# Kernel optimization log

Hardware: AMD Instinct MI355X
Metric: run time of the kernel (lower is better)

The kernel has to match this reference:

```python
import jax, jax.numpy as jnp
import numpy as np

B, S, HIDDEN = 2, 2048, 2048
H, KVH, HD = 16, 4, 128
N_REP = H // KVH
WIN = 3  # hardcoded window_size in the module
ROPE_THETA = 10000.0


def _rope(x, cos, sin):
    # x: [b, s, h, d]; cos/sin: [s, d//2]. Pairs are consecutive elements
    # (view_as_complex on reshape(..., -1, 2)): a = even idx, b = odd idx.
    a = x[..., 0::2]
    b = x[..., 1::2]
    c = cos[None, :, None, :]
    s = sin[None, :, None, :]
    out = jnp.stack([a * c - b * s, a * s + b * c], axis=-1)  # [b,s,h,d//2,2]
    return out.reshape(x.shape)


def setup_inputs() -> dict:
    key = jax.random.key(0)
    ks = jax.random.split(key, 5)
    x = jax.random.normal(ks[0], (B, S, HIDDEN), dtype=jnp.float32)
    scale = 0.02
    wq = jax.random.normal(ks[1], (HIDDEN, H * HD), dtype=jnp.float32) * scale
    wk = jax.random.normal(ks[2], (HIDDEN, KVH * HD), dtype=jnp.float32) * scale
    wv = jax.random.normal(ks[3], (HIDDEN, KVH * HD), dtype=jnp.float32) * scale
    wo = jax.random.normal(ks[4], (H * HD, HIDDEN), dtype=jnp.float32) * scale
    # Standard RoPE angles (equivalent to the complex freqs_cis)
    inv_freq = 1.0 / (ROPE_THETA ** (np.arange(0, HD, 2, dtype=np.float64) / HD))
    ang = np.outer(np.arange(S, dtype=np.float64), inv_freq)  # [S, HD//2]
    cos = jnp.asarray(np.cos(ang), dtype=jnp.float32)
    sin = jnp.asarray(np.sin(ang), dtype=jnp.float32)
    return {"x": x, "wq": wq, "wk": wk, "wv": wv, "wo": wo, "cos": cos, "sin": sin}


def reference(x, wq, wk, wv, wo, cos, sin):
    q = (x @ wq).reshape(B, S, H, HD)
    k = (x @ wk).reshape(B, S, KVH, HD)
    v = (x @ wv).reshape(B, S, KVH, HD)
    q = _rope(q, cos, sin)
    k = _rope(k, cos, sin)
    # GQA: repeat kv heads (repeat_kv)
    k = jnp.repeat(k, N_REP, axis=2)  # [B,S,H,HD]
    v = jnp.repeat(v, N_REP, axis=2)
    scores = jnp.einsum("bqhd,bkhd->bhqk", q, k) / np.float32(np.sqrt(HD))
    i = jnp.arange(S)[:, None]
    j = jnp.arange(S)[None, :]
    allowed = (j <= i) & (j > i - WIN)
    scores = jnp.where(allowed, scores, -jnp.inf)
    attn = jax.nn.softmax(scores.astype(jnp.float32), axis=-1).astype(q.dtype)
    out = jnp.einsum("bhqk,bkhd->bqhd", attn, v).reshape(B, S, H * HD)
    return (out @ wo, attn)
```

## Files before the change

### kernel.cpp

```cpp
#include <hip/hip_runtime.h>

#define SEQ 2048
#define HID 2048
#define NH 16
#define NKVH 4
#define HDIM 128
#define NB 2
#define MTOT (NB * SEQ)
#define QKV_N (NH * HDIM + 2 * NKVH * HDIM)
#define OUT0_ELEMS (NB * SEQ * HID)
#define ATTN_ELEMS ((size_t)NB * NH * SEQ * SEQ)
#define Z1_CHUNK 26048
#define Z1_TOTAL ((long)768 * Z1_CHUNK)
#define Z2_CHUNK 26464

typedef __bf16 bf16x8 __attribute__((ext_vector_type(8)));
typedef float f32x4 __attribute__((ext_vector_type(4)));

__device__ __forceinline__ unsigned short f2bf(float f) {
  unsigned int u = __float_as_uint(f);
  u += 0x7FFFu + ((u >> 16) & 1u);
  return (unsigned short)(u >> 16);
}
__device__ __forceinline__ float bf2f(unsigned short u) {
  return __uint_as_float(((unsigned int)u) << 16);
}

__global__ __launch_bounds__(256) void prep_k(
    const float* __restrict__ x, const float* __restrict__ wq,
    const float* __restrict__ wk, const float* __restrict__ wv,
    const float* __restrict__ wo, unsigned short* __restrict__ Xbf,
    unsigned short* __restrict__ Wqkvt, unsigned short* __restrict__ Wot) {
  __shared__ float tile[32][33];
  const int bid = blockIdx.x, t = threadIdx.x;
  if (bid < 8192) {
    int i = bid * 256 + t;
    float4 v = ((const float4*)x)[i];
    ushort4 o;
    o.x = f2bf(v.x); o.y = f2bf(v.y); o.z = f2bf(v.z); o.w = f2bf(v.w);
    ((ushort4*)Xbf)[i] = o;
    return;
  }
  int lb = bid - 8192;
  const float* W; unsigned short* Wt; int gx, N;
  if (lb < 4096)      { W = wq; Wt = Wqkvt;                       gx = 64; N = 2048; }
  else if (lb < 5120) { W = wk; Wt = Wqkvt + (size_t)2048 * HID;  gx = 16; N = 512;  lb -= 4096; }
  else if (lb < 6144) { W = wv; Wt = Wqkvt + (size_t)2560 * HID;  gx = 16; N = 512;  lb -= 5120; }
  else                { W = wo; Wt = Wot;                         gx = 64; N = 2048; lb -= 6144; }
  const int n0 = (lb % gx) * 32, k0 = (lb / gx) * 32;
  const int tx = t & 31, ty = t >> 5;
  #pragma unroll
  for (int r = 0; r < 32; r += 8)
    tile[ty + r][tx] = W[(size_t)(k0 + ty + r) * N + n0 + tx];
  __syncthreads();
  #pragma unroll
  for (int r = 0; r < 32; r += 8)
    Wt[(size_t)(n0 + ty + r) * HID + k0 + tx] = f2bf(tile[tx][ty + r]);
}

template <bool OUT_BF16>
__global__ __launch_bounds__(256) void gemm_bt_k(
    const unsigned short* __restrict__ A, const unsigned short* __restrict__ Bt,
    void* __restrict__ Cv, int M, int N, int K,
    f32x4* __restrict__ attn4, long zoff, int zchunk) {
  __shared__ unsigned short As[128 * 64];
  __shared__ unsigned short Bs[128 * 64];
  const int t = threadIdx.x;
  const int nbx = gridDim.x;
  const int rawbid = blockIdx.y * nbx + blockIdx.x;
  const int nwg = nbx * gridDim.y;
  const int sw = (rawbid & 7) * (nwg >> 3) + (rawbid >> 3);
  const int row0 = (sw / nbx) << 7;
  const int col0 = (sw % nbx) << 7;
  const int lane = t & 63;
  const int wave = t >> 6;
  const int wr = (wave >> 1) << 6;
  const int wc = (wave & 1) << 6;
  const int lrow = lane & 15;
  const int kofs = (lane >> 4) << 3;

  const long zbase = zoff + (long)rawbid * zchunk;

  f32x4 acc[4][4];
  #pragma unroll
  for (int a = 0; a < 4; ++a)
    #pragma unroll
    for (int b = 0; b < 4; ++b)
      #pragma unroll
      for (int r = 0; r < 4; ++r) acc[a][b][r] = 0.f;

  const unsigned short* Ab = A + (size_t)row0 * K;
  const unsigned short* Bb = Bt + (size_t)col0 * K;

  const int nk = K >> 6;
  for (int kt = 0; kt < nk; ++kt) {
    const int k0 = kt << 6;
    if (kt) __syncthreads();
    #pragma unroll
    for (int i = 0; i < 4; ++i) {
      const int c = i * 256 + t;
      const int row = c >> 3, c8 = (c & 7) << 3;
      __builtin_amdgcn_global_load_lds(
          (const __attribute__((address_space(1))) void*)(Ab + (size_t)row * K + k0 + c8),
          (__attribute__((address_space(3))) void*)(As + c * 8), 16, 0, 0);
      __builtin_amdgcn_global_load_lds(
          (const __attribute__((address_space(1))) void*)(Bb + (size_t)row * K + k0 + c8),
          (__attribute__((address_space(3))) void*)(Bs + c * 8), 16, 0, 0);
    }
    __syncthreads();

    #pragma unroll
    for (int s = 0; s < 4; ++s) {
      int il = (kt * 4 + s) * 256 + t;
      if (il < zchunk) {
        long g = zbase + il;
        int c = (int)(g & 511);
        int i = (int)((g >> 9) & (SEQ - 1));
        int hi = i >> 2;
        int lo = (i >= 2 ? i - 2 : 0) >> 2;
        if (c != hi && c != lo) {
          f32x4 z = {0.f, 0.f, 0.f, 0.f};
          __builtin_nontemporal_store(z, attn4 + g);
        }
      }
    }

    #pragma unroll
    for (int ks = 0; ks < 2; ++ks) {
      bf16x8 af[4], bfr[4];
      #pragma unroll
      for (int mf = 0; mf < 4; ++mf)
        af[mf] = *(const bf16x8*)(As + ((wr + mf * 16 + lrow) << 6) + (ks << 5) + kofs);
      #pragma unroll
      for (int nf = 0; nf < 4; ++nf)
        bfr[nf] = *(const bf16x8*)(Bs + ((wc + nf * 16 + lrow) << 6) + (ks << 5) + kofs);
      #pragma unroll
      for (int mf = 0; mf < 4; ++mf)
        #pragma unroll
        for (int nf = 0; nf < 4; ++nf)
          acc[mf][nf] = __builtin_amdgcn_mfma_f32_16x16x32_bf16(af[mf], bfr[nf],
                                                                acc[mf][nf], 0, 0, 0);
    }
  }

  const int cr = row0 + wr + ((lane >> 4) << 2);
  const int cc = col0 + wc + (lane & 15);
  #pragma unroll
  for (int mf = 0; mf < 4; ++mf)
    #pragma unroll
    for (int nf = 0; nf < 4; ++nf)
      #pragma unroll
      for (int r = 0; r < 4; ++r) {
        size_t idx = (size_t)(cr + mf * 16 + r) * N + cc + nf * 16;
        if constexpr (OUT_BF16)
          ((unsigned short*)Cv)[idx] = f2bf(acc[mf][nf][r]);
        else
          ((float*)Cv)[idx] = acc[mf][nf][r];
      }
}

__global__ void attn_k(const unsigned short* __restrict__ QKV,
                       unsigned short* __restrict__ AO,
                       float* __restrict__ attn_out,
                       const float* __restrict__ cosT,
                       const float* __restrict__ sinT) {
  int unit = blockIdx.x * 4 + (threadIdx.x >> 6);
  int lane = threadIdx.x & 63;
  int kh = unit & (NKVH - 1);
  int mi = unit >> 2;
  int i = mi & (SEQ - 1);
  int b = mi >> 11;
  const float SCALE = 0.08838834764831845f;

  float ci = cosT[i * 64 + lane], si = sinT[i * 64 + lane];

  float qa[4], qb[4];
  #pragma unroll
  for (int hh = 0; hh < 4; ++hh) {
    ushort2 qv = *(const ushort2*)(QKV + (size_t)mi * QKV_N + (kh * 4 + hh) * HDIM + 2 * lane);
    float a = bf2f(qv.x), bb = bf2f(qv.y);
    qa[hh] = a * ci - bb * si;
    qb[hh] = a * si + bb * ci;
  }

  float ka[3], kb[3], va[3], vb[3];
  #pragma unroll
  for (int jj = 0; jj < 3; ++jj) { ka[jj] = kb[jj] = va[jj] = vb[jj] = 0.f; }
  #pragma unroll
  for (int jj = 0; jj < 3; ++jj) {
    int j = i - 2 + jj;
    if (j >= 0) {
      const unsigned short* rp = QKV + (size_t)(mi - i + j) * QKV_N;
      float cj = cosT[j * 64 + lane], sj = sinT[j * 64 + lane];
      ushort2 kv = *(const ushort2*)(rp + 2048 + kh * HDIM + 2 * lane);
      float a = bf2f(kv.x), bb = bf2f(kv.y);
      ka[jj] = a * cj - bb * sj;
      kb[jj] = a * sj + bb * cj;
      ushort2 vv = *(const ushort2*)(rp + 2560 + kh * HDIM + 2 * lane);
      va[jj] = bf2f(vv.x); vb[jj] = bf2f(vv.y);
    }
  }

  float d[4][3];
  #pragma unroll
  for (int hh = 0; hh < 4; ++hh)
    #pragma unroll
    for (int jj = 0; jj < 3; ++jj) {
      int j = i - 2 + jj;
      float part = qa[hh] * ka[jj] + qb[hh] * kb[jj];
      #pragma unroll
      for (int o = 32; o; o >>= 1) part += __shfl_xor(part, o, 64);
      d[hh][jj] = (j >= 0) ? part * SCALE : -1e30f;
    }

  int rowb = (b * NH + kh * 4) * SEQ + i;
  int lo = (i >= 2 ? i - 2 : 0) >> 2;
  int hi = i >> 2;
  #pragma unroll
  for (int hh = 0; hh < 4; ++hh) {
    float mx = fmaxf(fmaxf(d[hh][0], d[hh][1]), d[hh][2]);
    float p0 = __expf(d[hh][0] - mx), p1 = __expf(d[hh][1] - mx), p2 = __expf(d[hh][2] - mx);
    float inv = 1.0f / (p0 + p1 + p2);
    float aw0 = p0 * inv, aw1 = p1 * inv, aw2 = p2 * inv;

    float oa = aw0 * va[0] + aw1 * va[1] + aw2 * va[2];
    float ob = aw0 * vb[0] + aw1 * vb[1] + aw2 * vb[2];
    ushort2 ov; ov.x = f2bf(oa); ov.y = f2bf(ob);
    *(ushort2*)(AO + (size_t)mi * HID + (kh * 4 + hh) * HDIM + 2 * lane) = ov;

    if (lane == 2 * hh || (lane == 2 * hh + 1 && hi != lo)) {
      int c = (lane == 2 * hh) ? lo : hi;
      f32x4 val = {0.f, 0.f, 0.f, 0.f};
      float aw[3] = {aw0, aw1, aw2};
      #pragma unroll
      for (int q = 0; q < 4; ++q) {
        int j = c * 4 + q;
        int dd = j - (i - 2);
        if (dd >= 0 && dd < 3 && j <= i) val[q] = aw[dd];
      }
      __builtin_nontemporal_store(
          val, (f32x4*)(attn_out + ((size_t)rowb + (size_t)hh * SEQ) * SEQ) + c);
    }
  }
}

extern "C" void kernel_launch(void* const* d_in, const int* in_sizes, int n_in,
                              void* d_out, int out_size, void* d_ws, size_t ws_size,
                              hipStream_t stream) {
  const float* x    = (const float*)d_in[0];
  const float* wq   = (const float*)d_in[1];
  const float* wk   = (const float*)d_in[2];
  const float* wv   = (const float*)d_in[3];
  const float* wo   = (const float*)d_in[4];
  const float* cosT = (const float*)d_in[5];
  const float* sinT = (const float*)d_in[6];

  float* out  = (float*)d_out;
  float* attn = out + OUT0_ELEMS;

  char* ws = (char*)d_ws;
  unsigned short* Xbf   = (unsigned short*)ws;  ws += (size_t)MTOT * HID * 2;
  unsigned short* Wqkvt = (unsigned short*)ws;  ws += (size_t)QKV_N * HID * 2;
  unsigned short* Wot   = (unsigned short*)ws;  ws += (size_t)HID * HID * 2;
  unsigned short* QKV   = (unsigned short*)ws;  ws += (size_t)MTOT * QKV_N * 2;
  unsigned short* AO    = (unsigned short*)ws;

  prep_k<<<18432, 256, 0, stream>>>(x, wq, wk, wv, wo, Xbf, Wqkvt, Wot);

  gemm_bt_k<true><<<dim3(QKV_N / 128, MTOT / 128), 256, 0, stream>>>(
      Xbf, Wqkvt, QKV, MTOT, QKV_N, HID, (f32x4*)attn, 0L, Z1_CHUNK);

  attn_k<<<MTOT * NKVH / 4, 256, 0, stream>>>(QKV, AO, attn, cosT, sinT);

  gemm_bt_k<false><<<dim3(HID / 128, MTOT / 128), 256, 0, stream>>>(
      AO, Wot, out, MTOT, HID, HID, (f32x4*)attn, Z1_TOTAL, Z2_CHUNK);
}
```

Before: 188.6 us.

## Double-buffer LDS tiles in bf16 GEMM to overlap global loads with MFMA

The GEMM kernel now keeps two LDS buffers for the A and B tiles. It issues the global_load_lds for tile k+1 before computing on tile k, and waits with an explicit s_waitcnt vmcnt so that only the newest prefetch may still be in flight. The goal is to hide global-memory latency behind the MFMA work, which the old single-buffer load-sync-compute loop exposed. In exchange, LDS use per block doubles to 64KB, which can reduce occupancy, and correctness now depends on hand-written vmcnt and barrier placement.

```diff
diff --git a/kernel.cpp b/kernel.cpp
--- a/kernel.cpp
+++ b/kernel.cpp
@@ -63,8 +63,8 @@
     const unsigned short* __restrict__ A, const unsigned short* __restrict__ Bt,
     void* __restrict__ Cv, int M, int N, int K,
     f32x4* __restrict__ attn4, long zoff, int zchunk) {
-  __shared__ unsigned short As[128 * 64];
-  __shared__ unsigned short Bs[128 * 64];
+  __shared__ unsigned short As[2][128 * 64];
+  __shared__ unsigned short Bs[2][128 * 64];
   const int t = threadIdx.x;
   const int nbx = gridDim.x;
   const int rawbid = blockIdx.y * nbx + blockIdx.x;
@@ -92,22 +92,35 @@
   const unsigned short* Ab = A + (size_t)row0 * K;
   const unsigned short* Bb = Bt + (size_t)col0 * K;
 
+#define STAGE(buf, k0)                                                         \
+  {                                                                            \
+    _Pragma("unroll")                                                          \
+    for (int i_ = 0; i_ < 4; ++i_) {                                           \
+      const int c_ = i_ * 256 + t;                                             \
+      const int row_ = c_ >> 3, co_ = (c_ & 7) << 3;                           \
+      __builtin_amdgcn_global_load_lds(                                        \
+          (const __attribute__((address_space(1))) void*)(Ab + (size_t)row_ * K + (k0) + co_), \
+          (__attribute__((address_space(3))) void*)(&As[buf][c_ * 8]), 16, 0, 0); \
+      __builtin_amdgcn_global_load_lds(                                        \
+          (const __attribute__((address_space(1))) void*)(Bb + (size_t)row_ * K + (k0) + co_), \
+          (__attribute__((address_space(3))) void*)(&Bs[buf][c_ * 8]), 16, 0, 0); \
+    }                                                                          \
+  }
+
   const int nk = K >> 6;
+  STAGE(0, 0)
+
   for (int kt = 0; kt < nk; ++kt) {
-    const int k0 = kt << 6;
-    if (kt) __syncthreads();
-    #pragma unroll
-    for (int i = 0; i < 4; ++i) {
-      const int c = i * 256 + t;
-      const int row = c >> 3, c8 = (c & 7) << 3;
-      __builtin_amdgcn_global_load_lds(
-          (const __attribute__((address_space(1))) void*)(Ab + (size_t)row * K + k0 + c8),
-          (__attribute__((address_space(3))) void*)(As + c * 8), 16, 0, 0);
-      __builtin_amdgcn_global_load_lds(
-          (const __attribute__((address_space(1))) void*)(Bb + (size_t)row * K + k0 + c8),
-          (__attribute__((address_space(3))) void*)(Bs + c * 8), 16, 0, 0);
-    }
-    __syncthreads();
+    const int cur = kt & 1;
+    if (kt + 1 < nk) {
+      STAGE(cur ^ 1, (kt + 1) << 6)
+      asm volatile("s_waitcnt vmcnt(8)" ::: "memory");
+    } else {
+      asm volatile("s_waitcnt vmcnt(0)" ::: "memory");
+    }
+    __builtin_amdgcn_sched_barrier(0);
+    __builtin_amdgcn_s_barrier();
+    __builtin_amdgcn_sched_barrier(0);
 
     #pragma unroll
     for (int s = 0; s < 4; ++s) {
@@ -130,10 +143,10 @@
       bf16x8 af[4], bfr[4];
       #pragma unroll
       for (int mf = 0; mf < 4; ++mf)
-        af[mf] = *(const bf16x8*)(As + ((wr + mf * 16 + lrow) << 6) + (ks << 5) + kofs);
+        af[mf] = *(const bf16x8*)(&As[cur][((wr + mf * 16 + lrow) << 6) + (ks << 5) + kofs]);
       #pragma unroll
       for (int nf = 0; nf < 4; ++nf)
-        bfr[nf] = *(const bf16x8*)(Bs + ((wc + nf * 16 + lrow) << 6) + (ks << 5) + kofs);
+        bfr[nf] = *(const bf16x8*)(&Bs[cur][((wc + nf * 16 + lrow) << 6) + (ks << 5) + kofs]);
       #pragma unroll
       for (int mf = 0; mf < 4; ++mf)
         #pragma unroll
@@ -141,7 +154,10 @@
           acc[mf][nf] = __builtin_amdgcn_mfma_f32_16x16x32_bf16(af[mf], bfr[nf],
                                                                 acc[mf][nf], 0, 0, 0);
     }
-  }
+    __builtin_amdgcn_sched_barrier(0);
+    __builtin_amdgcn_s_barrier();
+  }
+#undef STAGE
 
   const int cr = row0 + wr + ((lane >> 4) << 2);
   const int cc = col0 + wc + (lane & 15);
```

Result: slower. 222.2 us (+17.8%).
